# Performance work log

Hardware: AMD Instinct MI355X
Metric: run time of the kernel (lower is better)

The kernel has to match this reference:

```python
import jax, jax.numpy as jnp
import numpy as np

MAX_ATOMS = 13   # forward hard-codes x[:, :13, :]
LEN = 100        # ll1 output width, conv kernel = 2*LEN


def setup_inputs() -> dict:
    key = jax.random.key(0)
    k0, k1, k2, k3, k4 = jax.random.split(key, 5)
    B, S, d_model = 8192, 13, 512
    x = jax.random.normal(k0, (B, S, d_model), dtype=jnp.float32)
    # ll1: Linear(d_model, 100)
    W1 = jax.random.normal(k1, (LEN, d_model), dtype=jnp.float32) / np.sqrt(d_model)
    b1 = jax.random.normal(k2, (LEN,), dtype=jnp.float32) * 0.01
    # conv: Conv2d(1, 4, kernel=(1,200), stride=(1,200)) == per-pair linear 200->4
    Wc = jax.random.normal(k3, (4, 2 * LEN), dtype=jnp.float32) / np.sqrt(2 * LEN)
    bc = jax.random.normal(k4, (4,), dtype=jnp.float32) * 0.01
    return {"x": x, "W1": W1, "b1": b1, "Wc": Wc, "bc": bc, "max_atoms": MAX_ATOMS}


def reference(x, W1, b1, Wc, bc, max_atoms):
    # ll1 on first MAX_ATOMS atom embeddings -> [B, A, 100]
    feat = x[:, :MAX_ATOMS] @ W1.T + b1
    # pairwise ordered concat: block (i,j) = [feat[min(i,j)], feat[max(i,j)]]
    i = jnp.arange(max_atoms)[:, None]
    j = jnp.arange(max_atoms)[None, :]
    lo = jnp.minimum(i, j)   # [A, A]
    hi = jnpomaximum = jnp.maximum(i, j)
    pair = jnp.concatenate([feat[:, lo], feat[:, hi]], axis=-1)  # [B, A, A, 200]
    # stride==kernel Conv2d == batched linear over each 200-wide block -> [B, A, A, 4]
    # (matches final_e.permute(0, 2, 3, 1) layout)
    return jnp.einsum("bijc,oc->bijo", pair, Wc) + bc
```

## Files before the change

kernel.cpp:

```cpp
#include <hip/hip_runtime.h>
#include <hip/hip_bf16.h>


#define NA 13
#define DM 512
#define NOH 8

__global__ __launch_bounds__(512) void precompute_M(
    const float* __restrict__ W1, const float* __restrict__ b1,
    const float* __restrict__ Wc, const float* __restrict__ bc,
    float* __restrict__ M, float* __restrict__ s) {
    int oh = blockIdx.x;
    int o = oh & 3, half = oh >> 2;
    int d = threadIdx.x;
    const float* wc = Wc + o * 200 + half * 100;
    float acc = 0.f;
    for (int c = 0; c < 100; ++c)
        acc = fmaf(wc[c], W1[c * DM + d], acc);
    M[oh * DM + d] = acc;
    if (d == 0) {
        float sv = (half == 0) ? bc[o] : 0.f;
        for (int c = 0; c < 100; ++c) sv = fmaf(wc[c], b1[c], sv);
        s[oh] = sv;
    }
}

__global__ __launch_bounds__(256) void edge_main(
    const float* __restrict__ x, const float* __restrict__ M,
    const float* __restrict__ s, float* __restrict__ out) {
    const int b = blockIdx.x;
    const int lane = threadIdx.x & 63;
    const int wave = threadIdx.x >> 6;

    float4 mA[NOH], mB[NOH];
#pragma unroll
    for (int oh = 0; oh < NOH; ++oh) {
        mA[oh] = *(const float4*)(M + oh * DM + lane * 4);
        mB[oh] = *(const float4*)(M + oh * DM + 256 + lane * 4);
    }
    const float s_lane = s[lane & 7];

    const bool m1 = (lane & 1) != 0;
    const bool m2 = (lane & 2) != 0;
    const bool m4 = (lane & 4) != 0;

    __shared__ float G[NA][NOH];

    const float* xb = x + (size_t)b * (NA * DM);
#pragma unroll
    for (int k = 0; k < 4; ++k) {
        const int a = wave + 4 * k;
        if (a < NA) {
            float4 xA = *(const float4*)(xb + a * DM + lane * 4);
            float4 xB = *(const float4*)(xb + a * DM + 256 + lane * 4);
            float acc[NOH];
#pragma unroll
            for (int oh = 0; oh < NOH; ++oh) {
                float v = xA.x * mA[oh].x;
                v = fmaf(xA.y, mA[oh].y, v);
                v = fmaf(xA.z, mA[oh].z, v);
                v = fmaf(xA.w, mA[oh].w, v);
                v = fmaf(xB.x, mB[oh].x, v);
                v = fmaf(xB.y, mB[oh].y, v);
                v = fmaf(xB.z, mB[oh].z, v);
                v = fmaf(xB.w, mB[oh].w, v);
                acc[oh] = v;
            }
            float r1[4];
#pragma unroll
            for (int q = 0; q < 4; ++q) {
                float keep = m1 ? acc[2 * q + 1] : acc[2 * q];
                float send = m1 ? acc[2 * q]     : acc[2 * q + 1];
                r1[q] = keep + __shfl_xor(send, 1, 64);
            }
            float r2[2];
#pragma unroll
            for (int q = 0; q < 2; ++q) {
                float keep = m2 ? r1[2 * q + 1] : r1[2 * q];
                float send = m2 ? r1[2 * q]     : r1[2 * q + 1];
                r2[q] = keep + __shfl_xor(send, 2, 64);
            }
            {
                float keep = m4 ? r2[1] : r2[0];
                float send = m4 ? r2[0] : r2[1];
                float t = keep + __shfl_xor(send, 4, 64);
                t += __shfl_xor(t, 8, 64);
                t += __shfl_xor(t, 16, 64);
                t += __shfl_xor(t, 32, 64);
                if (lane < NOH) G[a][lane] = t + s_lane;
            }
        }
    }
    __syncthreads();

    const int t = threadIdx.x;
    if (t < NA * NA) {
        int i = t / NA, j = t % NA;
        int lo = i < j ? i : j;
        int hi = i < j ? j : i;
        float4 v;
        v.x = G[lo][0] + G[hi][4];
        v.y = G[lo][1] + G[hi][5];
        v.z = G[lo][2] + G[hi][6];
        v.w = G[lo][3] + G[hi][7];
        ((float4*)(out + (size_t)b * (NA * NA * 4)))[t] = v;
    }
}

extern "C" void kernel_launch(void* const* d_in, const int* in_sizes, int n_in,
                              void* d_out, int out_size, void* d_ws, size_t ws_size,
                              hipStream_t stream) {
    const float* x  = (const float*)d_in[0];
    const float* W1 = (const float*)d_in[1];
    const float* b1 = (const float*)d_in[2];
    const float* Wc = (const float*)d_in[3];
    const float* bc = (const float*)d_in[4];
    float* out = (float*)d_out;

    float* M = (float*)d_ws;
    float* s = M + NOH * DM;

    precompute_M<<<8, 512, 0, stream>>>(W1, b1, Wc, bc, M, s);
    edge_main<<<8192, 256, 0, stream>>>(x, M, s, out);
}
```

Measured before the change: 47.97 us.

## Make edge kernel persistent with double-buffered LDS and nontemporal loads/stores

Turns edge_main into a grid-stride persistent kernel over 2048 blocks. Each block loads the M weights into registers once and reuses them across many batch rows. The shared G buffer is double-buffered so each row needs only one barrier. Loads of x and stores of out use nontemporal builtins to avoid cache pollution, and precompute_M is split across more blocks. The batch count is derived from in_sizes[0], which is only correct if that value counts elements rather than bytes.

```diff
diff --git a/kernel.cpp b/kernel.cpp
--- a/kernel.cpp
+++ b/kernel.cpp
@@ -5,14 +5,17 @@
 #define NA 13
 #define DM 512
 #define NOH 8
+#define NBLK 2048
 
-__global__ __launch_bounds__(512) void precompute_M(
+typedef float fv4 __attribute__((ext_vector_type(4)));
+
+__global__ __launch_bounds__(128) void precompute_M(
     const float* __restrict__ W1, const float* __restrict__ b1,
     const float* __restrict__ Wc, const float* __restrict__ bc,
     float* __restrict__ M, float* __restrict__ s) {
     int oh = blockIdx.x;
     int o = oh & 3, half = oh >> 2;
-    int d = threadIdx.x;
+    int d = blockIdx.y * 128 + threadIdx.x;
     const float* wc = Wc + o * 200 + half * 100;
     float acc = 0.f;
     for (int c = 0; c < 100; ++c)
@@ -25,18 +28,17 @@
     }
 }
 
-__global__ __launch_bounds__(256) void edge_main(
+__global__ __launch_bounds__(256, 4) void edge_main(
     const float* __restrict__ x, const float* __restrict__ M,
-    const float* __restrict__ s, float* __restrict__ out) {
-    const int b = blockIdx.x;
+    const float* __restrict__ s, float* __restrict__ out, int B) {
     const int lane = threadIdx.x & 63;
     const int wave = threadIdx.x >> 6;
 
-    float4 mA[NOH], mB[NOH];
+    fv4 mA[NOH], mB[NOH];
 #pragma unroll
     for (int oh = 0; oh < NOH; ++oh) {
-        mA[oh] = *(const float4*)(M + oh * DM + lane * 4);
-        mB[oh] = *(const float4*)(M + oh * DM + 256 + lane * 4);
+        mA[oh] = *(const fv4*)(M + oh * DM + lane * 4);
+        mB[oh] = *(const fv4*)(M + oh * DM + 256 + lane * 4);
     }
     const float s_lane = s[lane & 7];
 
@@ -44,66 +46,70 @@
     const bool m2 = (lane & 2) != 0;
     const bool m4 = (lane & 4) != 0;
 
-    __shared__ float G[NA][NOH];
+    __shared__ float G[2][NA][NOH];
+    int p = 0;
 
-    const float* xb = x + (size_t)b * (NA * DM);
+    for (int b = blockIdx.x; b < B; b += NBLK) {
+        const float* xb = x + (size_t)b * (NA * DM);
 #pragma unroll
-    for (int k = 0; k < 4; ++k) {
-        const int a = wave + 4 * k;
-        if (a < NA) {
-            float4 xA = *(const float4*)(xb + a * DM + lane * 4);
-            float4 xB = *(const float4*)(xb + a * DM + 256 + lane * 4);
-            float acc[NOH];
+        for (int k = 0; k < 4; ++k) {
+            const int a = wave + 4 * k;
+            if (a < NA) {
+                fv4 xA = __builtin_nontemporal_load(
+                    (const fv4*)(xb + a * DM + lane * 4));
+                fv4 xB = __builtin_nontemporal_load(
+                    (const fv4*)(xb + a * DM + 256 + lane * 4));
+                float acc[NOH];
 #pragma unroll
-            for (int oh = 0; oh < NOH; ++oh) {
-                float v = xA.x * mA[oh].x;
-                v = fmaf(xA.y, mA[oh].y, v);
-                v = fmaf(xA.z, mA[oh].z, v);
-                v = fmaf(xA.w, mA[oh].w, v);
-                v = fmaf(xB.x, mB[oh].x, v);
-                v = fmaf(xB.y, mB[oh].y, v);
-                v = fmaf(xB.z, mB[oh].z, v);
-                v = fmaf(xB.w, mB[oh].w, v);
-                acc[oh] = v;
-            }
-            float r1[4];
+                for (int oh = 0; oh < NOH; ++oh) {
+                    float v = xA.x * mA[oh].x;
+                    v = fmaf(xA.y, mA[oh].y, v);
+                    v = fmaf(xA.z, mA[oh].z, v);
+                    v = fmaf(xA.w, mA[oh].w, v);
+                    v = fmaf(xB.x, mB[oh].x, v);
+                    v = fmaf(xB.y, mB[oh].y, v);
+                    v = fmaf(xB.z, mB[oh].z, v);
+                    v = fmaf(xB.w, mB[oh].w, v);
+                    acc[oh] = v;
+                }
+                float r1[4];
 #pragma unroll
-            for (int q = 0; q < 4; ++q) {
-                float keep = m1 ? acc[2 * q + 1] : acc[2 * q];
-                float send = m1 ? acc[2 * q]     : acc[2 * q + 1];
-                r1[q] = keep + __shfl_xor(send, 1, 64);
-            }
-            float r2[2];
+                for (int q = 0; q < 4; ++q) {
+                    float keep = m1 ? acc[2 * q + 1] : acc[2 * q];
+                    float send = m1 ? acc[2 * q]     : acc[2 * q + 1];
+                    r1[q] = keep + __shfl_xor(send, 1, 64);
+                }
+                float r2[2];
 #pragma unroll
-            for (int q = 0; q < 2; ++q) {
-                float keep = m2 ? r1[2 * q + 1] : r1[2 * q];
-                float send = m2 ? r1[2 * q]     : r1[2 * q + 1];
-                r2[q] = keep + __shfl_xor(send, 2, 64);
-            }
-            {
+                for (int q = 0; q < 2; ++q) {
+                    float keep = m2 ? r1[2 * q + 1] : r1[2 * q];
+                    float send = m2 ? r1[2 * q]     : r1[2 * q + 1];
+                    r2[q] = keep + __shfl_xor(send, 2, 64);
+                }
                 float keep = m4 ? r2[1] : r2[0];
                 float send = m4 ? r2[0] : r2[1];
                 float t = keep + __shfl_xor(send, 4, 64);
                 t += __shfl_xor(t, 8, 64);
                 t += __shfl_xor(t, 16, 64);
                 t += __shfl_xor(t, 32, 64);
-                if (lane < NOH) G[a][lane] = t + s_lane;
+                if (lane < NOH) G[p][a][lane] = t + s_lane;
             }
         }
-    }
-    __syncthreads();
-
-    const int t = threadIdx.x;
-    if (t < NA * NA) {
-        int i = t / NA, j = t % NA;
-        int lo = i < j ? i : j;
-        int hi = i < j ? j : i;
-        float4 v;
-        v.x = G[lo][0] + G[hi][4];
-        v.y = G[lo][1] + G[hi][5];
-        v.z = G[lo][2] + G[hi][6];
-        v.w = G[lo][3] + G[hi][7];
-        ((float4*)(out + (size_t)b * (NA * NA * 4)))[t] = v;
+        __syncthreads();
+        const int t = threadIdx.x;
+        if (t < NA * NA) {
+            int i = t / NA, j = t % NA;
+            int lo = i < j ? i : j;
+            int hi = i < j ? j : i;
+            fv4 v;
+            v.x = G[p][lo][0] + G[p][hi][4];
+            v.y = G[p][lo][1] + G[p][hi][5];
+            v.z = G[p][lo][2] + G[p][hi][6];
+            v.w = G[p][lo][3] + G[p][hi][7];
+            __builtin_nontemporal_store(
+                v, (fv4*)(out + (size_t)b * (NA * NA * 4)) + t);
+        }
+        p ^= 1;
     }
 }
 
@@ -116,10 +122,11 @@
     const float* Wc = (const float*)d_in[3];
     const float* bc = (const float*)d_in[4];
     float* out = (float*)d_out;
+    const int B = in_sizes[0] / (NA * DM);
 
     float* M = (float*)d_ws;
     float* s = M + NOH * DM;
 
-    precompute_M<<<8, 512, 0, stream>>>(W1, b1, Wc, bc, M, s);
-    edge_main<<<8192, 256, 0, stream>>>(x, M, s, out);
+    precompute_M<<<dim3(8, 4), 128, 0, stream>>>(W1, b1, Wc, bc, M, s);
+    edge_main<<<NBLK, 256, 0, stream>>>(x, M, s, out, B);
 }
```

Result: slower. 54.42 us (+13.4%).
